# Kernel tuning notes

Measured on AMD Instinct MI355X. Metric: run time of the kernel, lower is better.

The kernel has to match this reference:

```python
import jax, jax.numpy as jnp
import numpy as np

NUM_HEADS = 16
HEAD_DIM = 64
TAU = 0.07
EPS = 1e-12  # torch F.normalize eps


def setup_inputs() -> dict:
    key = jax.random.key(0)
    ks = jax.random.split(key, 12)
    B, L, D = 4, 2048, 1024
    s = 1.0 / np.sqrt(D)
    inp = {
        'q': jax.random.normal(ks[0], (B, L, D), jnp.float32),
        'k': jax.random.normal(ks[1], (B, L, D), jnp.float32),
        'v': jax.random.normal(ks[2], (B, L, D), jnp.float32),
        'Wq': jax.random.normal(ks[3], (D, D), jnp.float32) * s,
        'bq': jax.random.normal(ks[4], (D,), jnp.float32) * 0.01,
        'Wk': jax.random.normal(ks[5], (D, D), jnp.float32) * s,
        'bk': jax.random.normal(ks[6], (D,), jnp.float32) * 0.01,
        'Wv': jax.random.normal(ks[7], (D, D), jnp.float32) * s,
        'bv': jax.random.normal(ks[8], (D,), jnp.float32) * 0.01,
        'Wo': jax.random.normal(ks[9], (D, D), jnp.float32) * s,
        'bo': jax.random.normal(ks[10], (D,), jnp.float32) * 0.01,
    }
    return inp


def _split(x):
    b, l, d = x.shape
    return x.reshape(b, l, NUM_HEADS, HEAD_DIM).transpose(0, 2, 1, 3)  # [b,h,l,dh]


def _l2norm(x):
    n = jnp.sqrt(jnp.sum(x * x, axis=-1, keepdims=True))
    return x / jnp.maximum(n, EPS)


def reference(q, k, v, Wq, bq, Wk, bk, Wv, bv, Wo, bo):
    # Linear projections (torch Linear: y = x @ W.T + b)
    qh = _l2norm(_split(q @ Wq.T + bq))
    kh = _l2norm(_split(k @ Wk.T + bk))
    vh = _split(v @ Wv.T + bv)
    scores = jnp.einsum('bhqd,bhkd->bhqk', qh, kh) / max(TAU, 1e-6)
    attn = jax.nn.softmax(scores, axis=-1)  # dropout = identity in eval
    out = jnp.einsum('bhqk,bhkd->bhqd', attn, vh)
    b, h, l, dh = out.shape
    merged = out.transpose(0, 2, 1, 3).reshape(b, l, h * dh)
    return merged @ Wo.T + bo
```

## Files before the change

### kernel.cpp

```cpp
#include <hip/hip_runtime.h>

#define BB 4
#define LL 2048
#define DD 1024
#define NH 16
#define DH 64
#define MM (BB*LL)

typedef _Float16 half8 __attribute__((ext_vector_type(8)));
typedef _Float16 half4 __attribute__((ext_vector_type(4)));
typedef _Float16 half2 __attribute__((ext_vector_type(2)));
typedef float floatx4 __attribute__((ext_vector_type(4)));

__device__ __forceinline__ void gload_lds16(const void* g, void* l) {
    __builtin_amdgcn_global_load_lds((const __attribute__((address_space(1))) void*)g,
                                     (__attribute__((address_space(3))) void*)l,
                                     16, 0, 0);
}

__device__ __forceinline__ floatx4 mfma16(half8 a, half8 b, floatx4 c) {
    return __builtin_amdgcn_mfma_f32_16x16x32_f16(a, b, c, 0, 0, 0);
}

__global__ __launch_bounds__(256) void cvt_all(const float* __restrict__ q,
                                               const float* __restrict__ k,
                                               const float* __restrict__ v,
                                               const float* __restrict__ Wq,
                                               const float* __restrict__ Wk,
                                               const float* __restrict__ Wv,
                                               const float* __restrict__ Wo,
                                               _Float16* __restrict__ dst) {
    const int BIG = 8192;
    const int SML = 1024;
    const size_t NQKV = (size_t)MM * DD;
    const size_t NW = (size_t)DD * DD;
    int b = blockIdx.x;
    const float* src;
    size_t off;
    int lb;
    if (b < 3 * BIG) {
        int t = b / BIG;
        src = t == 0 ? q : (t == 1 ? k : v);
        off = (size_t)t * NQKV;
        lb = b - t * BIG;
    } else {
        int t = (b - 3 * BIG) / SML;
        src = t == 0 ? Wq : (t == 1 ? Wk : (t == 2 ? Wv : Wo));
        off = 3 * NQKV + (size_t)t * NW;
        lb = b - 3 * BIG - t * SML;
    }
    size_t i = (size_t)lb * 256 + threadIdx.x;
    float4 f = ((const float4*)src)[i];
    half4 h;
    h[0] = (_Float16)f.x; h[1] = (_Float16)f.y;
    h[2] = (_Float16)f.z; h[3] = (_Float16)f.w;
    ((half4*)(dst + off))[i] = h;
}

__global__ __launch_bounds__(256) void gemm_qkv(const _Float16* __restrict__ qkv16,
                                                const _Float16* __restrict__ wq,
                                                const _Float16* __restrict__ wk,
                                                const _Float16* __restrict__ wv,
                                                const float* __restrict__ bq,
                                                const float* __restrict__ bk,
                                                const float* __restrict__ bv,
                                                _Float16* __restrict__ Qp,
                                                _Float16* __restrict__ Kp,
                                                _Float16* __restrict__ VtG) {
    const int K = 1024;
    __shared__ _Float16 As[128 * 32];
    __shared__ _Float16 Bs[128 * 32];

    int tid = threadIdx.x;
    int wave = tid >> 6, lane = tid & 63;
    int quad = lane >> 4, l15 = lane & 15;
    int wrow = (wave >> 1) * 64, wcol = (wave & 1) * 64;
    int bx = blockIdx.x;
    int which = bx >> 3;
    int m0 = blockIdx.y * 128;
    int n0 = (bx & 7) * 128;

    const _Float16* A = qkv16 + (size_t)which * ((size_t)MM * DD);
    const _Float16* W = which == 0 ? wq : (which == 1 ? wk : wv);
    const float* bias = which == 0 ? bq : (which == 1 ? bk : bv);

    floatx4 acc[4][4] = {};

    int srow = tid >> 2, sseg = tid & 3;
    const _Float16* Ag0 = A + (size_t)(m0 + srow) * K + sseg * 8;
    const _Float16* Ag1 = Ag0 + (size_t)64 * K;
    const _Float16* Bg0 = W + (size_t)(n0 + srow) * K + sseg * 8;
    const _Float16* Bg1 = Bg0 + (size_t)64 * K;
    char* ldsA0 = (char*)As + tid * 16;
    char* ldsA1 = (char*)As + (256 + tid) * 16;
    char* ldsB0 = (char*)Bs + tid * 16;
    char* ldsB1 = (char*)Bs + (256 + tid) * 16;

    for (int kt = 0; kt < K; kt += 32) {
        __syncthreads();
        gload_lds16(Ag0 + kt, ldsA0);
        gload_lds16(Ag1 + kt, ldsA1);
        gload_lds16(Bg0 + kt, ldsB0);
        gload_lds16(Bg1 + kt, ldsB1);
        __syncthreads();

        half8 af[4], bf[4];
#pragma unroll
        for (int i = 0; i < 4; i++)
            af[i] = *(half8*)&As[(wrow + i * 16 + l15) * 32 + quad * 8];
#pragma unroll
        for (int j = 0; j < 4; j++)
            bf[j] = *(half8*)&Bs[(wcol + j * 16 + l15) * 32 + quad * 8];
#pragma unroll
        for (int i = 0; i < 4; i++)
#pragma unroll
            for (int j = 0; j < 4; j++)
                acc[i][j] = mfma16(af[i], bf[j], acc[i][j]);
    }

#pragma unroll
    for (int j = 0; j < 4; j++) {
        float bv_ = bias[n0 + wcol + j * 16 + l15];
#pragma unroll
        for (int i = 0; i < 4; i++)
#pragma unroll
            for (int r = 0; r < 4; r++) acc[i][j][r] += bv_;
    }

    if (which < 2) {
        _Float16* C = which == 0 ? Qp : Kp;
#pragma unroll
        for (int i = 0; i < 4; i++) {
#pragma unroll
            for (int r = 0; r < 4; r++) {
                float s = 0.f;
#pragma unroll
                for (int j = 0; j < 4; j++) s += acc[i][j][r] * acc[i][j][r];
                s += __shfl_xor(s, 1);
                s += __shfl_xor(s, 2);
                s += __shfl_xor(s, 4);
                s += __shfl_xor(s, 8);
                float inv = 1.0f / fmaxf(sqrtf(s), 1e-12f);
                int row = m0 + wrow + i * 16 + quad * 4 + r;
#pragma unroll
                for (int j = 0; j < 4; j++) {
                    int col = n0 + wcol + j * 16 + l15;
                    C[(size_t)row * DD + col] = (_Float16)(acc[i][j][r] * inv);
                }
            }
        }
    } else {
#pragma unroll
        for (int j = 0; j < 4; j++) {
            int col = n0 + wcol + j * 16 + l15;
#pragma unroll
            for (int i = 0; i < 4; i++) {
#pragma unroll
                for (int r = 0; r < 4; r++) {
                    int row = m0 + wrow + i * 16 + quad * 4 + r;
                    int b = row >> 11, l = row & 2047;
                    VtG[((size_t)((b << 10) + col)) * LL + l] = (_Float16)acc[i][j][r];
                }
            }
        }
    }
}

__global__ __launch_bounds__(256) void gemm_out(const _Float16* __restrict__ A,
                                                const _Float16* __restrict__ W,
                                                const float* __restrict__ bias,
                                                float* __restrict__ C) {
    const int K = 1024, N = 1024;
    __shared__ _Float16 As[128 * 32];
    __shared__ _Float16 Bs[128 * 32];

    int tid = threadIdx.x;
    int wave = tid >> 6, lane = tid & 63;
    int quad = lane >> 4, l15 = lane & 15;
    int wrow = (wave >> 1) * 64, wcol = (wave & 1) * 64;
    int m0 = blockIdx.y * 128;
    int n0 = blockIdx.x * 128;

    floatx4 acc[4][4] = {};

    int srow = tid >> 2, sseg = tid & 3;
    const _Float16* Ag0 = A + (size_t)(m0 + srow) * K + sseg * 8;
    const _Float16* Ag1 = Ag0 + (size_t)64 * K;
    const _Float16* Bg0 = W + (size_t)(n0 + srow) * K + sseg * 8;
    const _Float16* Bg1 = Bg0 + (size_t)64 * K;
    char* ldsA0 = (char*)As + tid * 16;
    char* ldsA1 = (char*)As + (256 + tid) * 16;
    char* ldsB0 = (char*)Bs + tid * 16;
    char* ldsB1 = (char*)Bs + (256 + tid) * 16;

    for (int kt = 0; kt < K; kt += 32) {
        __syncthreads();
        gload_lds16(Ag0 + kt, ldsA0);
        gload_lds16(Ag1 + kt, ldsA1);
        gload_lds16(Bg0 + kt, ldsB0);
        gload_lds16(Bg1 + kt, ldsB1);
        __syncthreads();

        half8 af[4], bf[4];
#pragma unroll
        for (int i = 0; i < 4; i++)
            af[i] = *(half8*)&As[(wrow + i * 16 + l15) * 32 + quad * 8];
#pragma unroll
        for (int j = 0; j < 4; j++)
            bf[j] = *(half8*)&Bs[(wcol + j * 16 + l15) * 32 + quad * 8];
#pragma unroll
        for (int i = 0; i < 4; i++)
#pragma unroll
            for (int j = 0; j < 4; j++)
                acc[i][j] = mfma16(af[i], bf[j], acc[i][j]);
    }

#pragma unroll
    for (int j = 0; j < 4; j++) {
        int col = n0 + wcol + j * 16 + l15;
        float bv = bias[col];
#pragma unroll
        for (int i = 0; i < 4; i++) {
#pragma unroll
            for (int r = 0; r < 4; r++) {
                int row = m0 + wrow + i * 16 + quad * 4 + r;
                C[(size_t)row * N + col] = acc[i][j][r] + bv;
            }
        }
    }
}

__global__ __launch_bounds__(256) void attn_k(const _Float16* __restrict__ Q,
                                              const _Float16* __restrict__ K,
                                              const _Float16* __restrict__ VtG,
                                              _Float16* __restrict__ Mg) {
    __shared__ _Float16 Ks[64 * 64];
    __shared__ _Float16 Vt[64 * 64];
    __shared__ _Float16 Ps[128 * 64];
    __shared__ float lsum[128];

    const float C2 = 20.60992915555662f;
    const float OFF = 6.0f;

    int tid = threadIdx.x, wave = tid >> 6, lane = tid & 63;
    int quad = lane >> 4, l15 = lane & 15;
    int bh = blockIdx.y;
    int b = bh >> 4, h = bh & 15;
    int q0 = blockIdx.x * 128;
    size_t rowBase = (size_t)b * LL;
    int colBase = h * 64;
    int wq = wave * 32;
    int sw = l15 & 7;

    half8 qf[2][2];
#pragma unroll
    for (int ib = 0; ib < 2; ib++)
#pragma unroll
        for (int ks = 0; ks < 2; ks++)
            qf[ib][ks] = *(const half8*)(Q + (rowBase + q0 + wq + ib * 16 + l15) * DD +
                                         colBase + ks * 32 + quad * 8);

    const _Float16* kg[2];
    const _Float16* vg[2];
    char* kl[2];
    char* vl[2];
#pragma unroll
    for (int p = 0; p < 2; p++) {
        int s = p * 256 + tid;
        int r = s >> 3, cs = s & 7;
        int ck = cs ^ (r & 7);
        kg[p] = K + (rowBase + r) * DD + colBase + ck * 8;
        kl[p] = (char*)Ks + s * 16;
        vg[p] = VtG + ((size_t)bh * 64 + r) * LL + ck * 8;
        vl[p] = (char*)Vt + s * 16;
    }

    floatx4 oacc[2][4] = {};
    float fsum[2] = {0.f, 0.f};

    for (int kt = 0; kt < LL; kt += 64) {
        __syncthreads();
        gload_lds16(kg[0], kl[0]); kg[0] += 64 * DD;
        gload_lds16(kg[1], kl[1]); kg[1] += 64 * DD;
        gload_lds16(vg[0], vl[0]); vg[0] += 64;
        gload_lds16(vg[1], vl[1]); vg[1] += 64;
        __syncthreads();

        floatx4 st[2][4] = {};
#pragma unroll
        for (int ks = 0; ks < 2; ks++) {
            half8 kf[4];
#pragma unroll
            for (int jb = 0; jb < 4; jb++)
                kf[jb] = *(half8*)&Ks[(jb * 16 + l15) * 64 + (((ks * 4 + quad) ^ sw) * 8)];
#pragma unroll
            for (int ib = 0; ib < 2; ib++)
#pragma unroll
                for (int jb = 0; jb < 4; jb++)
                    st[ib][jb] = mfma16(kf[jb], qf[ib][ks], st[ib][jb]);
        }

#pragma unroll
        for (int ib = 0; ib < 2; ib++) {
#pragma unroll
            for (int jb = 0; jb < 4; jb++) {
                float e0 = __builtin_amdgcn_exp2f(st[ib][jb][0] * C2 - OFF);
                float e1 = __builtin_amdgcn_exp2f(st[ib][jb][1] * C2 - OFF);
                float e2 = __builtin_amdgcn_exp2f(st[ib][jb][2] * C2 - OFF);
                float e3 = __builtin_amdgcn_exp2f(st[ib][jb][3] * C2 - OFF);
                fsum[ib] += (e0 + e1) + (e2 + e3);
                half2 p01 = __builtin_bit_cast(half2, __builtin_amdgcn_cvt_pkrtz(e0, e1));
                half2 p23 = __builtin_bit_cast(half2, __builtin_amdgcn_cvt_pkrtz(e2, e3));
                half4 pk; pk[0] = p01[0]; pk[1] = p01[1]; pk[2] = p23[0]; pk[3] = p23[1];
                int chunk = (jb * 2 + (quad >> 1)) ^ sw;
                *(half4*)((char*)Ps + (wq + ib * 16 + l15) * 128 + chunk * 16 + (quad & 1) * 8) = pk;
            }
        }

#pragma unroll
        for (int kb = 0; kb < 2; kb++) {
            half8 pf[2];
#pragma unroll
            for (int ib = 0; ib < 2; ib++)
                pf[ib] = *(half8*)&Ps[(wq + ib * 16 + l15) * 64 + (((kb * 4 + quad) ^ sw) * 8)];
#pragma unroll
            for (int jb = 0; jb < 4; jb++) {
                half8 vf = *(half8*)&Vt[(jb * 16 + l15) * 64 + (((kb * 4 + quad) ^ sw) * 8)];
#pragma unroll
                for (int ib = 0; ib < 2; ib++)
                    oacc[ib][jb] = mfma16(pf[ib], vf, oacc[ib][jb]);
            }
        }
    }

#pragma unroll
    for (int ib = 0; ib < 2; ib++) {
        float v = fsum[ib];
        v += __shfl_xor(v, 16);
        v += __shfl_xor(v, 32);
        lsum[wq + ib * 16 + l15] = v;
    }
#pragma unroll
    for (int ib = 0; ib < 2; ib++) {
#pragma unroll
        for (int r = 0; r < 4; r++) {
            float inv = 1.0f / lsum[wq + ib * 16 + quad * 4 + r];
            int qrow = q0 + wq + ib * 16 + quad * 4 + r;
#pragma unroll
            for (int jb = 0; jb < 4; jb++) {
                float v = oacc[ib][jb][r] * inv;
                Mg[(rowBase + qrow) * DD + colBase + jb * 16 + l15] = (_Float16)v;
            }
        }
    }
}

extern "C" void kernel_launch(void* const* d_in, const int* in_sizes, int n_in,
                              void* d_out, int out_size, void* d_ws, size_t ws_size,
                              hipStream_t stream) {
    (void)in_sizes; (void)n_in; (void)out_size; (void)ws_size;
    const float* q  = (const float*)d_in[0];
    const float* k  = (const float*)d_in[1];
    const float* v  = (const float*)d_in[2];
    const float* Wq = (const float*)d_in[3];
    const float* bq = (const float*)d_in[4];
    const float* Wk = (const float*)d_in[5];
    const float* bk = (const float*)d_in[6];
    const float* Wv = (const float*)d_in[7];
    const float* bv = (const float*)d_in[8];
    const float* Wo = (const float*)d_in[9];
    const float* bo = (const float*)d_in[10];

    const size_t NQKV = (size_t)MM * DD;
    const size_t NW = (size_t)DD * DD;

    _Float16* q16  = (_Float16*)d_ws;
    _Float16* k16  = q16 + NQKV;
    _Float16* v16  = k16 + NQKV;
    _Float16* wq16 = v16 + NQKV;
    _Float16* wk16 = wq16 + NW;
    _Float16* wv16 = wk16 + NW;
    _Float16* wo16 = wv16 + NW;
    _Float16* Qp   = wo16 + NW;
    _Float16* Kp   = Qp + NQKV;
    _Float16* VtG  = Kp + NQKV;
    _Float16* Mg   = VtG + NQKV;
    (void)k16; (void)v16;

    cvt_all<<<dim3(3 * 8192 + 4 * 1024), dim3(256), 0, stream>>>(q, k, v, Wq, Wk, Wv, Wo, q16);

    gemm_qkv<<<dim3(24, MM / 128), dim3(256), 0, stream>>>(q16, wq16, wk16, wv16,
                                                           bq, bk, bv, Qp, Kp, VtG);

    attn_k<<<dim3(LL / 128, BB * NH), dim3(256), 0, stream>>>(Qp, Kp, VtG, Mg);

    gemm_out<<<dim3(1024 / 128, MM / 128), dim3(256), 0, stream>>>(Mg, wo16, bo, (float*)d_out);
}
```

Measured before the change: 373.5 us.

## Rewrite attention with 32x32 MFMA, register-resident P, and double-buffered K/V

The attention kernel moves from 16x16x32 to 32x32x16 MFMA tiles. The probability tile P is now rearranged in registers with permlane32_swap, so it no longer makes a round trip through a shared-memory staging buffer. K and V tiles are double-buffered in LDS and the next tile's async global-to-LDS load is issued before computing on the current one, which removes one barrier per iteration. s_setprio hints are also added around the MFMA blocks. The cost is more LDS for the doubled buffers, larger accumulators and more register pressure, and a permlane builtin that ties the kernel to specific gfx targets.

Measured after the change: 372.7 us. No clear change (-0.2%).

```diff
diff --git a/kernel.cpp b/kernel.cpp
--- a/kernel.cpp
+++ b/kernel.cpp
@@ -11,6 +11,8 @@
 typedef _Float16 half4 __attribute__((ext_vector_type(4)));
 typedef _Float16 half2 __attribute__((ext_vector_type(2)));
 typedef float floatx4 __attribute__((ext_vector_type(4)));
+typedef float floatx16 __attribute__((ext_vector_type(16)));
+typedef unsigned uint4v __attribute__((ext_vector_type(4)));
 
 __device__ __forceinline__ void gload_lds16(const void* g, void* l) {
     __builtin_amdgcn_global_load_lds((const __attribute__((address_space(1))) void*)g,
@@ -20,6 +22,14 @@
 
 __device__ __forceinline__ floatx4 mfma16(half8 a, half8 b, floatx4 c) {
     return __builtin_amdgcn_mfma_f32_16x16x32_f16(a, b, c, 0, 0, 0);
+}
+
+__device__ __forceinline__ floatx16 mfma32(half8 a, half8 b, floatx16 c) {
+    return __builtin_amdgcn_mfma_f32_32x32x16_f16(a, b, c, 0, 0, 0);
+}
+
+__device__ __forceinline__ unsigned pkh(float a, float b) {
+    return __builtin_bit_cast(unsigned, __builtin_amdgcn_cvt_pkrtz(a, b));
 }
 
 __global__ __launch_bounds__(256) void cvt_all(const float* __restrict__ q,
@@ -234,123 +244,137 @@
                                               const _Float16* __restrict__ K,
                                               const _Float16* __restrict__ VtG,
                                               _Float16* __restrict__ Mg) {
-    __shared__ _Float16 Ks[64 * 64];
-    __shared__ _Float16 Vt[64 * 64];
-    __shared__ _Float16 Ps[128 * 64];
+    __shared__ _Float16 Ks[2][64 * 64];
+    __shared__ _Float16 Vt[2][64 * 64];
     __shared__ float lsum[128];
 
     const float C2 = 20.60992915555662f;
     const float OFF = 6.0f;
 
     int tid = threadIdx.x, wave = tid >> 6, lane = tid & 63;
-    int quad = lane >> 4, l15 = lane & 15;
+    int l31 = lane & 31, hi = lane >> 5;
     int bh = blockIdx.y;
     int b = bh >> 4, h = bh & 15;
     int q0 = blockIdx.x * 128;
     size_t rowBase = (size_t)b * LL;
     int colBase = h * 64;
     int wq = wave * 32;
-    int sw = l15 & 7;
-
-    half8 qf[2][2];
-#pragma unroll
-    for (int ib = 0; ib < 2; ib++)
-#pragma unroll
-        for (int ks = 0; ks < 2; ks++)
-            qf[ib][ks] = *(const half8*)(Q + (rowBase + q0 + wq + ib * 16 + l15) * DD +
-                                         colBase + ks * 32 + quad * 8);
+    int xorv = l31 & 7;
+
+    half8 qf[4];
+    const _Float16* qp = Q + (rowBase + q0 + wq + l31) * DD + colBase + hi * 8;
+#pragma unroll
+    for (int d = 0; d < 4; d++) qf[d] = *(const half8*)(qp + d * 16);
 
     const _Float16* kg[2];
     const _Float16* vg[2];
-    char* kl[2];
-    char* vl[2];
+    int ldso[2];
 #pragma unroll
     for (int p = 0; p < 2; p++) {
         int s = p * 256 + tid;
-        int r = s >> 3, cs = s & 7;
-        int ck = cs ^ (r & 7);
-        kg[p] = K + (rowBase + r) * DD + colBase + ck * 8;
-        kl[p] = (char*)Ks + s * 16;
-        vg[p] = VtG + ((size_t)bh * 64 + r) * LL + ck * 8;
-        vl[p] = (char*)Vt + s * 16;
-    }
-
-    floatx4 oacc[2][4] = {};
-    float fsum[2] = {0.f, 0.f};
-
-    for (int kt = 0; kt < LL; kt += 64) {
+        int r = s >> 3, cp = s & 7;
+        int cs = cp ^ (r & 7);
+        kg[p] = K + (rowBase + r) * DD + colBase + cs * 8;
+        vg[p] = VtG + ((size_t)bh * 64 + r) * LL + cs * 8;
+        ldso[p] = s * 16;
+    }
+
+    floatx16 oacc[2] = {};
+    float fsum = 0.f;
+
+    gload_lds16(kg[0], (char*)Ks[0] + ldso[0]);
+    gload_lds16(kg[1], (char*)Ks[0] + ldso[1]);
+    gload_lds16(vg[0], (char*)Vt[0] + ldso[0]);
+    gload_lds16(vg[1], (char*)Vt[0] + ldso[1]);
+    kg[0] += 64 * DD; kg[1] += 64 * DD; vg[0] += 64; vg[1] += 64;
+    __syncthreads();
+
+#pragma unroll 2
+    for (int kt = 0; kt < LL / 64; kt++) {
+        int cur = kt & 1;
+        if (kt + 1 < LL / 64) {
+            gload_lds16(kg[0], (char*)Ks[cur ^ 1] + ldso[0]);
+            gload_lds16(kg[1], (char*)Ks[cur ^ 1] + ldso[1]);
+            gload_lds16(vg[0], (char*)Vt[cur ^ 1] + ldso[0]);
+            gload_lds16(vg[1], (char*)Vt[cur ^ 1] + ldso[1]);
+            kg[0] += 64 * DD; kg[1] += 64 * DD; vg[0] += 64; vg[1] += 64;
+        }
+        const char* kb_ = (const char*)Ks[cur];
+        const char* vb_ = (const char*)Vt[cur];
+
+#pragma unroll
+        for (int c = 0; c < 2; c++) {
+            floatx16 st = {};
+            __builtin_amdgcn_s_setprio(1);
+#pragma unroll
+            for (int d = 0; d < 4; d++) {
+                half8 kf = *(const half8*)(kb_ + c * 4096 + l31 * 128 +
+                                           (((d * 2 + hi) ^ xorv) * 16));
+                st = mfma32(kf, qf[d], st);
+            }
+            __builtin_amdgcn_s_setprio(0);
+
+            float e[16];
+#pragma unroll
+            for (int r = 0; r < 16; r++)
+                e[r] = __builtin_amdgcn_exp2f(st[r] * C2 - OFF);
+
+            float s0 = (e[0] + e[1]) + (e[2] + e[3]);
+            float s1 = (e[4] + e[5]) + (e[6] + e[7]);
+            float s2 = (e[8] + e[9]) + (e[10] + e[11]);
+            float s3 = (e[12] + e[13]) + (e[14] + e[15]);
+            fsum += (s0 + s1) + (s2 + s3);
+
+            half8 pf[2];
+#pragma unroll
+            for (int sl = 0; sl < 2; sl++) {
+                int bse = sl * 8;
+                unsigned a = pkh(e[bse + 0], e[bse + 1]);
+                unsigned cc = pkh(e[bse + 2], e[bse + 3]);
+                unsigned bb = pkh(e[bse + 4], e[bse + 5]);
+                unsigned dd = pkh(e[bse + 6], e[bse + 7]);
+                auto r1 = __builtin_amdgcn_permlane32_swap(a, bb, false, false);
+                auto r2 = __builtin_amdgcn_permlane32_swap(cc, dd, false, false);
+                uint4v u;
+                u[0] = (unsigned)r1[0]; u[1] = (unsigned)r2[0];
+                u[2] = (unsigned)r1[1]; u[3] = (unsigned)r2[1];
+                pf[sl] = __builtin_bit_cast(half8, u);
+            }
+
+            __builtin_amdgcn_s_setprio(1);
+#pragma unroll
+            for (int jb = 0; jb < 2; jb++) {
+#pragma unroll
+                for (int sl = 0; sl < 2; sl++) {
+                    half8 vf = *(const half8*)(vb_ + jb * 4096 + l31 * 128 +
+                                               (((c * 4 + sl * 2 + hi) ^ xorv) * 16));
+                    oacc[jb] = mfma32(pf[sl], vf, oacc[jb]);
+                }
+            }
+            __builtin_amdgcn_s_setprio(0);
+        }
+
         __syncthreads();
-        gload_lds16(kg[0], kl[0]); kg[0] += 64 * DD;
-        gload_lds16(kg[1], kl[1]); kg[1] += 64 * DD;
-        gload_lds16(vg[0], vl[0]); vg[0] += 64;
-        gload_lds16(vg[1], vl[1]); vg[1] += 64;
-        __syncthreads();
-
-        floatx4 st[2][4] = {};
-#pragma unroll
-        for (int ks = 0; ks < 2; ks++) {
-            half8 kf[4];
-#pragma unroll
-            for (int jb = 0; jb < 4; jb++)
-                kf[jb] = *(half8*)&Ks[(jb * 16 + l15) * 64 + (((ks * 4 + quad) ^ sw) * 8)];
-#pragma unroll
-            for (int ib = 0; ib < 2; ib++)
-#pragma unroll
-                for (int jb = 0; jb < 4; jb++)
-                    st[ib][jb] = mfma16(kf[jb], qf[ib][ks], st[ib][jb]);
-        }
-
-#pragma unroll
-        for (int ib = 0; ib < 2; ib++) {
-#pragma unroll
-            for (int jb = 0; jb < 4; jb++) {
-                float e0 = __builtin_amdgcn_exp2f(st[ib][jb][0] * C2 - OFF);
-                float e1 = __builtin_amdgcn_exp2f(st[ib][jb][1] * C2 - OFF);
-                float e2 = __builtin_amdgcn_exp2f(st[ib][jb][2] * C2 - OFF);
-                float e3 = __builtin_amdgcn_exp2f(st[ib][jb][3] * C2 - OFF);
-                fsum[ib] += (e0 + e1) + (e2 + e3);
-                half2 p01 = __builtin_bit_cast(half2, __builtin_amdgcn_cvt_pkrtz(e0, e1));
-                half2 p23 = __builtin_bit_cast(half2, __builtin_amdgcn_cvt_pkrtz(e2, e3));
-                half4 pk; pk[0] = p01[0]; pk[1] = p01[1]; pk[2] = p23[0]; pk[3] = p23[1];
-                int chunk = (jb * 2 + (quad >> 1)) ^ sw;
-                *(half4*)((char*)Ps + (wq + ib * 16 + l15) * 128 + chunk * 16 + (quad & 1) * 8) = pk;
-            }
-        }
-
-#pragma unroll
-        for (int kb = 0; kb < 2; kb++) {
-            half8 pf[2];
-#pragma unroll
-            for (int ib = 0; ib < 2; ib++)
-                pf[ib] = *(half8*)&Ps[(wq + ib * 16 + l15) * 64 + (((kb * 4 + quad) ^ sw) * 8)];
-#pragma unroll
-            for (int jb = 0; jb < 4; jb++) {
-                half8 vf = *(half8*)&Vt[(jb * 16 + l15) * 64 + (((kb * 4 + quad) ^ sw) * 8)];
-#pragma unroll
-                for (int ib = 0; ib < 2; ib++)
-                    oacc[ib][jb] = mfma16(pf[ib], vf, oacc[ib][jb]);
-            }
-        }
-    }
-
-#pragma unroll
-    for (int ib = 0; ib < 2; ib++) {
-        float v = fsum[ib];
-        v += __shfl_xor(v, 16);
-        v += __shfl_xor(v, 32);
-        lsum[wq + ib * 16 + l15] = v;
-    }
-#pragma unroll
-    for (int ib = 0; ib < 2; ib++) {
-#pragma unroll
-        for (int r = 0; r < 4; r++) {
-            float inv = 1.0f / lsum[wq + ib * 16 + quad * 4 + r];
-            int qrow = q0 + wq + ib * 16 + quad * 4 + r;
-#pragma unroll
-            for (int jb = 0; jb < 4; jb++) {
-                float v = oacc[ib][jb][r] * inv;
-                Mg[(rowBase + qrow) * DD + colBase + jb * 16 + l15] = (_Float16)v;
-            }
+    }
+
+    fsum += __shfl_xor(fsum, 32);
+    lsum[wq + l31] = fsum;
+    __syncthreads();
+
+    float inv[16];
+#pragma unroll
+    for (int r = 0; r < 16; r++) {
+        int crow = (r & 3) + 8 * (r >> 2) + 4 * hi;
+        inv[r] = 1.0f / lsum[wq + crow];
+    }
+
+    _Float16* mp = Mg + (rowBase + q0 + wq) * DD + colBase + l31;
+#pragma unroll
+    for (int jb = 0; jb < 2; jb++) {
+#pragma unroll
+        for (int r = 0; r < 16; r++) {
+            int crow = (r & 3) + 8 * (r >> 2) + 4 * hi;
+            mp[(size_t)crow * DD + jb * 32] = (_Float16)(oacc[jb][r] * inv[r]);
         }
     }
 }
```
